# Optimization experiments

Hardware: AMD Instinct MI355X
Metric: run time of the kernel (lower is better)

The kernel has to match this reference:

```python
import jax, jax.numpy as jnp
import numpy as np

B, N = 128, 512            # graphs per batch, nodes (seq len) per graph
NODE_VOCAB, APP_VOCAB = 30000, 5000
D, R, K = 128, 512, 3      # embed_size, rec_embed dim, Chebyshev order
EPS = 1e-12


def setup_inputs() -> dict:
    key = jax.random.key(0)
    ks = jax.random.split(key, 8)
    return {
        # all tokens nonzero -> every position is a valid node (item > 0 filter passes)
        "input_seq": jax.random.randint(ks[0], (B, N), 1, NODE_VOCAB),
        "recd_token": jax.random.randint(ks[1], (B, N), 1, APP_VOCAB),
        "embed_table": jax.random.normal(ks[2], (NODE_VOCAB, D), jnp.float32) * 0.02,
        "rec_embed_table": jax.random.normal(ks[3], (APP_VOCAB, R), jnp.float32) * 0.02,
        "cheb_w1": jax.random.normal(ks[4], (K, D, D), jnp.float32) / np.sqrt(D),
        "cheb_b1": jnp.zeros((D,), jnp.float32),
        "cheb_w2": jax.random.normal(ks[5], (K, D, D), jnp.float32) / np.sqrt(D),
        "cheb_b2": jnp.zeros((D,), jnp.float32),
    }


def _prop_matrix(app_emb):
    """Per-sample scaled Laplacian L_hat = -D^{-1/2} A D^{-1/2}.

    app_emb: [B,N,R] (detached upstream, matching recd.detach() in the source).
    Adjacency: cosine-sim matrix, entries below the mean of the nonzero strict
    upper triangle zeroed. ChebConv receives edge_index only -> binary weights,
    self-loops removed, default lambda_max=2 -> L_hat = -A_norm.
    """
    app_feat = app_emb / jnp.maximum(
        jnp.linalg.norm(app_emb, axis=-1, keepdims=True), EPS)      # F.normalize dim=1
    A = jnp.einsum('bnr,bmr->bnm', app_feat, app_feat)              # [B,N,N]
    upper = jnp.triu(A, 1)
    cnt = jnp.sum(upper != 0, axis=(1, 2)).astype(A.dtype)
    mean = jnp.sum(upper, axis=(1, 2)) / jnp.maximum(cnt, 1.0)      # [B]
    A = jnp.where(A < mean[:, None, None], 0.0, A)
    adj = (A != 0).astype(A.dtype) * (1.0 - jnp.eye(N, dtype=A.dtype))  # binary, no self-loops
    deg = adj.sum(-1)                                               # [B,N]
    dinv = jnp.where(deg > 0, jax.lax.rsqrt(jnp.maximum(deg, EPS)), 0.0)
    return -(dinv[:, :, None] * adj * dinv[:, None, :])             # [B,N,N]


def _cheb(x, S, w, b):
    # Chebyshev recurrence T0=x, T1=Sx, T2=2S T1 - T0
    tx0 = x
    tx1 = jnp.einsum('bnm,bmd->bnd', S, tx0)
    tx2 = 2.0 * jnp.einsum('bnm,bmd->bnd', S, tx1) - tx0
    return (jnp.einsum('bnd,de->bne', tx0, w[0])
            + jnp.einsum('bnd,de->bne', tx1, w[1])
            + jnp.einsum('bnd,de->bne', tx2, w[2]) + b)


def reference(input_seq, recd_token, embed_table, rec_embed_table,
              cheb_w1, cheb_b1, cheb_w2, cheb_b2):
    app_emb = rec_embed_table[recd_token]                           # [B,N,R]
    # adjacency built from detached embeddings (recd.detach() in source)
    S = jax.lax.stop_gradient(_prop_matrix(jax.lax.stop_gradient(app_emb)))
    x = embed_table[input_seq]                                      # [B,N,D]
    x = jax.nn.relu(_cheb(x, S, cheb_w1, cheb_b1))
    x = jax.nn.relu(_cheb(x, S, cheb_w2, cheb_b2))
    out = jnp.concatenate([x, app_emb], axis=-1)                    # [B,N,D+R]
    return out.reshape(B * N, D + R)                                # Batch'ed node features
```

## Files before the change

### kernel.cpp

```cpp
#include <hip/hip_runtime.h>
#include <hip/hip_bf16.h>

typedef __attribute__((ext_vector_type(8))) unsigned short ushort8;
typedef __attribute__((ext_vector_type(4))) unsigned short bf16x4;
typedef __attribute__((ext_vector_type(8))) short short8;
typedef __attribute__((ext_vector_type(4))) float f32x4;
typedef __attribute__((ext_vector_type(2))) unsigned long long u64x2;

#define DEV __device__ __forceinline__

DEV unsigned short f2bf(float f) {
    unsigned u = __builtin_bit_cast(unsigned, f);
    return (unsigned short)((u + 0x7fffu + ((u >> 16) & 1u)) >> 16);
}
DEV float bf2f(unsigned short h) {
    unsigned u = ((unsigned)h) << 16;
    return __builtin_bit_cast(float, u);
}
DEV float wred(float v) {
#pragma unroll
    for (int m = 32; m > 0; m >>= 1) v += __shfl_xor(v, m, 64);
    return v;
}

constexpr int N_ = 512, D_ = 128, R_ = 512;
constexpr long NN2 = (long)N_ * N_;
constexpr int PSTR = 520;
constexpr int USTR = 136;

DEV void gll16(const void* g, void* l) {
    __builtin_amdgcn_global_load_lds(
        (const __attribute__((address_space(1))) unsigned*)g,
        (__attribute__((address_space(3))) unsigned*)l, 16, 0, 0);
}


__global__ __launch_bounds__(256) void k_front(const int* __restrict__ recd,
                                               const float* __restrict__ rtab,
                                               const int* __restrict__ seq,
                                               const float* __restrict__ etab,
                                               const float* __restrict__ w1,
                                               const float* __restrict__ w2,
                                               float* __restrict__ out,
                                               unsigned short* __restrict__ x,
                                               unsigned short* __restrict__ wT,
                                               unsigned short* __restrict__ rtb,
                                               float* __restrict__ rnorm) {
    int bid = blockIdx.x, tid = threadIdx.x;
    if (bid < 16384) {
        int lane = tid & 63, w = tid >> 6;
        long r = (long)bid * 4 + w;
        int tok = recd[r];
        const float* src = rtab + (long)tok * R_;
        int j = lane * 8;
        float4 v0 = *(const float4*)(src + j);
        float4 v1 = *(const float4*)(src + j + 4);
        float ssq = v0.x*v0.x + v0.y*v0.y + v0.z*v0.z + v0.w*v0.w
                  + v1.x*v1.x + v1.y*v1.y + v1.z*v1.z + v1.w*v1.w;
        ssq = wred(ssq);
        float* o = out + r * 640 + 128 + j;
        *(float4*)o = v0;
        *(float4*)(o + 4) = v1;
        if (lane == 0) rnorm[r] = 1.0f / fmaxf(sqrtf(ssq), 1e-12f);
    } else if (bid < 20480) {
        long e8 = ((long)(bid - 16384) * 256 + tid) * 8;
        long r = e8 >> 7;
        int d0 = (int)(e8 & 127);
        int tok = seq[r];
        const float* src = etab + (long)tok * D_ + d0;
        float4 v0 = *(const float4*)src, v1 = *(const float4*)(src + 4);
        ushort8 u;
        u[0]=f2bf(v0.x); u[1]=f2bf(v0.y); u[2]=f2bf(v0.z); u[3]=f2bf(v0.w);
        u[4]=f2bf(v1.x); u[5]=f2bf(v1.y); u[6]=f2bf(v1.z); u[7]=f2bf(v1.w);
        *(ushort8*)(x + e8) = u;
    } else if (bid < 20864) {
        int o = (bid - 20480) * 256 + tid;
        int l = o / 49152;
        int rr = o - l * 49152;
        int mat = rr >> 14;
        int e2 = rr & 16383;
        int e = e2 >> 7, d = e2 & 127;
        const float* w = l ? w2 : w1;
        float v;
        if (mat == 0)      v = w[d * 128 + e] - w[32768 + d * 128 + e];
        else if (mat == 1) v = w[16384 + d * 128 + e];
        else               v = 2.0f * w[32768 + d * 128 + e];
        wT[o] = f2bf(v);
    } else {
        long e8 = ((long)(bid - 20864) * 256 + tid) * 8;
        float4 v0 = *(const float4*)(rtab + e8), v1 = *(const float4*)(rtab + e8 + 4);
        ushort8 u;
        u[0]=f2bf(v0.x); u[1]=f2bf(v0.y); u[2]=f2bf(v0.z); u[3]=f2bf(v0.w);
        u[4]=f2bf(v1.x); u[5]=f2bf(v1.y); u[6]=f2bf(v1.z); u[7]=f2bf(v1.w);
        *(ushort8*)(rtb + e8) = u;
    }
}


DEV void stage_rowmajor(const unsigned short* base, long ld, int k0,
                        unsigned short* dst, int tid) {
#pragma unroll
    for (int i = 0; i < 4; ++i) {
        int u = i * 256 + tid;
        int r = u >> 3, c = (u & 7) * 8;
        gll16(base + (long)r * ld + k0 + c,
              dst + i * 2048 + (tid & 448) * 8);
    }
}

DEV void stage_gather(const unsigned short* tab, const int* toks, int k0,
                      unsigned short* dst, int tid) {
#pragma unroll
    for (int i = 0; i < 4; ++i) {
        int u = i * 256 + tid;
        int r = u >> 3, c = (u & 7) * 8;
        gll16(tab + (long)toks[r] * 512 + k0 + c,
              dst + i * 2048 + (tid & 448) * 8);
    }
}


DEV void stageA256(const unsigned short* base, int k0, unsigned short* dst, int tid) {
    int w = tid >> 6;
#pragma unroll
    for (int i = 0; i < 4; ++i) {
        int u = i * 512 + tid;
        int r = u >> 3, c = (u & 7) * 8;
        gll16(base + (long)r * 128 + k0 + c, dst + (i * 64 + w * 8) * 64);
    }
}

DEV void stageB128(const unsigned short* base, int k0, unsigned short* dst, int tid) {
    int w = tid >> 6;
#pragma unroll
    for (int i = 0; i < 2; ++i) {
        int u = i * 512 + tid;
        int r = u >> 3, c = (u & 7) * 8;
        gll16(base + (long)r * 128 + k0 + c, dst + (i * 64 + w * 8) * 64);
    }
}


__global__ __launch_bounds__(256) void k_adj(const unsigned short* __restrict__ rtb,
                                             const int* __restrict__ recd,
                                             const float* __restrict__ rnorm,
                                             unsigned short* __restrict__ Abf,
                                             float* __restrict__ psum,
                                             float* __restrict__ pcnt) {
    __shared__ __align__(16) unsigned short As[128 * 64], Bs[128 * 64];
    __shared__ int toks[256];
    __shared__ float sred[4], cred[4];
    int g = blockIdx.x;
    int r8 = g & 7, q = g >> 3;
    int q10 = q / 10;
    int b = r8 + (q10 << 3);
    int t = q - q10 * 10;
    int tm = (t < 4) ? 0 : (t < 7) ? 1 : (t < 9) ? 2 : 3;
    int tn = t - (tm * (9 - tm)) / 2 + tm;
    bool diag = (tm == tn);
    int tid = threadIdx.x, lane = tid & 63, wave = tid >> 6;
    if (tid < 128) toks[tid] = recd[b * 512 + tm * 128 + tid];
    else           toks[tid] = recd[b * 512 + tn * 128 + (tid - 128)];
    int wm = wave >> 1, wn = wave & 1;
    int fr = lane & 15, ko = (lane >> 4) * 8;
    f32x4 acc[4][4] = {};
    for (int k0 = 0; k0 < 512; k0 += 64) {
        __syncthreads();
        stage_gather(rtb, toks, k0, As, tid);
        if (!diag) stage_gather(rtb, toks + 128, k0, Bs, tid);
        __syncthreads();
        const unsigned short* Bsrc = diag ? As : Bs;
#pragma unroll
        for (int ks = 0; ks < 2; ++ks) {
            short8 a[4], bb[4];
#pragma unroll
            for (int m = 0; m < 4; ++m)
                a[m] = *(const short8*)(As + (wm * 64 + m * 16 + fr) * 64 + ks * 32 + ko);
#pragma unroll
            for (int n = 0; n < 4; ++n)
                bb[n] = *(const short8*)(Bsrc + (wn * 64 + n * 16 + fr) * 64 + ks * 32 + ko);
#pragma unroll
            for (int m = 0; m < 4; ++m)
#pragma unroll
                for (int n = 0; n < 4; ++n)
                    acc[m][n] = __builtin_amdgcn_mfma_f32_16x16x32_bf16(
                        a[m], bb[n], acc[m][n], 0, 0, 0);
        }
    }
    float s = 0.f, c = 0.f;
    unsigned short* Ab = Abf + (long)b * NN2;
    const float* rnb = rnorm + (long)b * 512;
#pragma unroll
    for (int m = 0; m < 4; ++m) {
        int gi0 = tm * 128 + wm * 64 + m * 16 + (lane >> 4) * 4;
        float4 rni = *(const float4*)(rnb + gi0);
#pragma unroll
        for (int n = 0; n < 4; ++n) {
            int gj = tn * 128 + wn * 64 + n * 16 + fr;
            float rj = rnb[gj];
            f32x4 v = acc[m][n];
            bf16x4 tw;
#pragma unroll
            for (int qq = 0; qq < 4; ++qq) {
                int gi = gi0 + qq;
                float vv = v[qq] * (&rni.x)[qq] * rj;
                unsigned short bv = f2bf(vv);
                Ab[(long)gi * N_ + gj] = bv;
                tw[qq] = bv;
                if (gj > gi) {
                    s += vv;
                    c += (vv != 0.0f) ? 1.0f : 0.0f;
                }
            }
            if (!diag)
                *(bf16x4*)(Ab + (long)gj * N_ + gi0) = tw;
        }
    }
    s = wred(s);
    c = wred(c);
    if (lane == 0) { sred[wave] = s; cred[wave] = c; }
    __syncthreads();
    if (tid == 0) {
        psum[b * 16 + t] = sred[0] + sred[1] + sred[2] + sred[3];
        pcnt[b * 16 + t] = cred[0] + cred[1] + cred[2] + cred[3];
    }
}

__global__ __launch_bounds__(256) void k_degtrs(unsigned short* __restrict__ Abf,
                                                const float* __restrict__ psum,
                                                const float* __restrict__ pcnt,
                                                const unsigned short* __restrict__ xin,
                                                float* __restrict__ dinv,
                                                unsigned short* __restrict__ pT) {
    __shared__ unsigned char mb[4][64];
    __shared__ float sdinv[64];
    __shared__ unsigned short t[64 * 128];
    int bid = blockIdx.x;
    int q = bid >> 3, r8 = bid & 7;
    int b = r8 + ((q >> 3) << 3);
    int tn = q & 7;
    int tid = threadIdx.x, lane = tid & 63, w = tid >> 6;
    float s = 0.f, c = 0.f;
#pragma unroll
    for (int k = 0; k < 10; ++k) { s += psum[b * 16 + k]; c += pcnt[b * 16 + k]; }
    float m = s / fmaxf(c, 1.0f);
#pragma unroll 1
    for (int i = 0; i < 16; ++i) {
        int rl = w * 16 + i;
        long r = (long)b * 512 + tn * 64 + rl;
        int ig = tn * 64 + rl;
        ushort8 v = *(const ushort8*)(Abf + r * 512 + lane * 8);
        unsigned byt = 0;
        int cnt = 0;
#pragma unroll
        for (int k = 0; k < 8; ++k) {
            float f = bf2f(v[k]);
            int j = lane * 8 + k;
            bool keep = (f >= m) && (f != 0.0f) && (j != ig);
            byt |= (keep ? 1u : 0u) << k;
            cnt += keep ? 1 : 0;
        }
        mb[w][lane] = (unsigned char)byt;
        float fc = wred((float)cnt);
        if (lane < 8) {
            unsigned long long mword = *(const unsigned long long*)&mb[w][lane * 8];
            *(unsigned long long*)((unsigned char*)Abf + r * 1024 + lane * 8) = mword;
        }
        if (lane == 8) {
            float dv = (fc > 0.f) ? rsqrtf(fc) : 0.f;
            dinv[r] = dv;
            sdinv[rl] = dv;
        }
    }
    __syncthreads();
    const unsigned short* ib = xin + ((long)b * 512 + tn * 64) * 128;
    unsigned short* ob = pT + (long)b * 65536 + tn * 64;
#pragma unroll
    for (int i = 0; i < 4; ++i) {
        int u = i * 256 + tid;
        int n = u >> 4, g = u & 15;
        float sc = sdinv[n];
        ushort8 v = *(const ushort8*)(ib + n * 128 + g * 8);
        ushort8 sv;
#pragma unroll
        for (int tt = 0; tt < 8; ++tt) sv[tt] = f2bf(bf2f(v[tt]) * sc);
        int gs = g ^ ((n >> 3) & 7);
        *(ushort8*)(t + n * 128 + gs * 8) = sv;
    }
    __syncthreads();
#pragma unroll
    for (int i = 0; i < 4; ++i) {
        int u = i * 256 + tid;
        int d = u >> 3, n8 = (u & 7) * 8;
        ushort8 v;
#pragma unroll
        for (int tt = 0; tt < 8; ++tt) {
            int n = n8 + tt;
            int g = (d >> 3) ^ ((n >> 3) & 7);
            v[tt] = t[n * 128 + g * 8 + (d & 7)];
        }
        *(ushort8*)(ob + (long)d * 512 + n8) = v;
    }
}

__global__ __launch_bounds__(512) void k_sxm(const unsigned short* __restrict__ Abf,
                                             const float* __restrict__ dinv,
                                             const unsigned short* __restrict__ pT,
                                             unsigned short* __restrict__ outN,
                                             unsigned short* __restrict__ outT) {
    __shared__ __align__(16) unsigned short Ps[128 * PSTR];
    __shared__ __align__(8) unsigned short lut4[16 * 4];
    int tid = threadIdx.x, lane = tid & 63, w = tid >> 6;
    if (tid < 16) {
        unsigned long long e = 0;
#pragma unroll
        for (int j = 0; j < 4; ++j)
            if ((tid >> j) & 1) e |= 0x3F80ull << (16 * j);
        *(unsigned long long*)(lut4 + tid * 4) = e;
    }
    int g = blockIdx.x;
    int xcd = g & 7, idx = g >> 3;
    int b = xcd + ((idx >> 1) << 3);
    int half = idx & 1;
    int wm = w >> 1, wn = w & 1;
    int fr = lane & 15, ko = (lane >> 4) * 8;
    const unsigned char* mbase = (const unsigned char*)Abf + (long)b * 524288;
    const unsigned short* pb = pT + (long)b * 65536;
#pragma unroll
    for (int i = 0; i < 16; ++i) {
        int r = i * 8 + w;
        gll16(pb + (long)r * 512 + lane * 8, Ps + r * PSTR);
    }
    __syncthreads();
    f32x4 acc[4][4] = {};
    int rowbase = half * 256 + wm * 64;
#pragma unroll 1
    for (int k0 = 0; k0 < 512; k0 += 128) {
        u64x2 mw[4];
#pragma unroll
        for (int m = 0; m < 4; ++m) {
            int row = rowbase + m * 16 + fr;
            mw[m] = *(const u64x2*)(mbase + (long)row * 1024 + (k0 >> 3));
        }
#pragma unroll
        for (int kss = 0; kss < 4; ++kss) {
            short8 a4[4], b4[4];
#pragma unroll
            for (int m = 0; m < 4; ++m) {
                unsigned w32 = (unsigned)(mw[m][kss >> 1] >> ((kss & 1) * 32));
                unsigned byt = (w32 >> ko) & 255u;
                unsigned long long lo = *(const unsigned long long*)(lut4 + (byt & 15u) * 4);
                unsigned long long hi = *(const unsigned long long*)(lut4 + (byt >> 4) * 4);
                u64x2 tt; tt[0] = lo; tt[1] = hi;
                a4[m] = __builtin_bit_cast(short8, tt);
            }
#pragma unroll
            for (int n = 0; n < 4; ++n)
                b4[n] = *(const short8*)(Ps + (wn * 64 + n * 16 + fr) * PSTR + k0 + kss * 32 + ko);
#pragma unroll
            for (int m = 0; m < 4; ++m)
#pragma unroll
                for (int n = 0; n < 4; ++n)
                    acc[m][n] = __builtin_amdgcn_mfma_f32_16x16x32_bf16(
                        a4[m], b4[n], acc[m][n], 0, 0, 0);
        }
    }
    unsigned short* on = outN + (long)b * 65536;
#pragma unroll
    for (int m = 0; m < 4; ++m) {
        int gi0 = half * 256 + wm * 64 + m * 16 + ((lane >> 4) << 2);
        float4 dv = *(const float4*)(dinv + (long)b * 512 + gi0);
#pragma unroll
        for (int n = 0; n < 4; ++n) {
            int gj = wn * 64 + n * 16 + fr;
            bf16x4 tw;
#pragma unroll
            for (int qq = 0; qq < 4; ++qq) {
                float dq = (&dv.x)[qq];
                float t1v = -dq * acc[m][n][qq];
                on[(long)(gi0 + qq) * 128 + gj] = f2bf(t1v);
                tw[qq] = f2bf(dq * t1v);
            }
            *(bf16x4*)(outT + (long)b * 65536 + (long)gj * 512 + gi0) = tw;
        }
    }
}

template <int LAYER>
__global__ __launch_bounds__(512) void k_sxp(const unsigned short* __restrict__ Abf,
                                             const float* __restrict__ dinv,
                                             const unsigned short* __restrict__ pTin,
                                             const unsigned short* __restrict__ t0,
                                             const unsigned short* __restrict__ t1,
                                             const unsigned short* __restrict__ wTl,
                                             const float* __restrict__ bias,
                                             unsigned short* __restrict__ ybf,
                                             unsigned short* __restrict__ pTout,
                                             float* __restrict__ out) {
    __shared__ __align__(16) unsigned short lds[128 * PSTR];
    __shared__ __align__(8) unsigned short lut4[16 * 4];
    int tid = threadIdx.x, lane = tid & 63, w = tid >> 6;
    if (tid < 16) {
        unsigned long long e = 0;
#pragma unroll
        for (int j = 0; j < 4; ++j)
            if ((tid >> j) & 1) e |= 0x3F80ull << (16 * j);
        *(unsigned long long*)(lut4 + tid * 4) = e;
    }
    int g = blockIdx.x;
    int xcd = g & 7, idx = g >> 3;
    int b = xcd + ((idx >> 1) << 3);
    int half = idx & 1;
    int wm = w >> 1, wn = w & 1;
    int fr = lane & 15, ko = (lane >> 4) * 8;
    unsigned short* As  = lds;
    unsigned short* Bs  = lds + 16384;
    unsigned short* uL  = lds + 24576;
    {
        const unsigned char* mbase = (const unsigned char*)Abf + (long)b * 524288;
        const unsigned short* pb = pTin + (long)b * 65536;
#pragma unroll
        for (int i = 0; i < 16; ++i) {
            int r = i * 8 + w;
            gll16(pb + (long)r * 512 + lane * 8, lds + r * PSTR);
        }
        __syncthreads();
        f32x4 acc[4][4] = {};
        int rowbase = half * 256 + wm * 64;
#pragma unroll 1
        for (int k0 = 0; k0 < 512; k0 += 128) {
            u64x2 mw[4];
#pragma unroll
            for (int m = 0; m < 4; ++m) {
                int row = rowbase + m * 16 + fr;
                mw[m] = *(const u64x2*)(mbase + (long)row * 1024 + (k0 >> 3));
            }
#pragma unroll
            for (int kss = 0; kss < 4; ++kss) {
                short8 a4[4], b4[4];
#pragma unroll
                for (int m = 0; m < 4; ++m) {
                    unsigned w32 = (unsigned)(mw[m][kss >> 1] >> ((kss & 1) * 32));
                    unsigned byt = (w32 >> ko) & 255u;
                    unsigned long long lo = *(const unsigned long long*)(lut4 + (byt & 15u) * 4);
                    unsigned long long hi = *(const unsigned long long*)(lut4 + (byt >> 4) * 4);
                    u64x2 tt; tt[0] = lo; tt[1] = hi;
                    a4[m] = __builtin_bit_cast(short8, tt);
                }
#pragma unroll
                for (int n = 0; n < 4; ++n)
                    b4[n] = *(const short8*)(lds + (wn * 64 + n * 16 + fr) * PSTR + k0 + kss * 32 + ko);
#pragma unroll
                for (int m = 0; m < 4; ++m)
#pragma unroll
                    for (int n = 0; n < 4; ++n)
                        acc[m][n] = __builtin_amdgcn_mfma_f32_16x16x32_bf16(
                            a4[m], b4[n], acc[m][n], 0, 0, 0);
            }
        }
        __syncthreads();
#pragma unroll
        for (int m = 0; m < 4; ++m) {
            int li0 = wm * 64 + m * 16 + ((lane >> 4) << 2);
            float4 dv = *(const float4*)(dinv + (long)b * 512 + half * 256 + li0);
#pragma unroll
            for (int n = 0; n < 4; ++n) {
                int gj = wn * 64 + n * 16 + fr;
#pragma unroll
                for (int qq = 0; qq < 4; ++qq)
                    uL[(li0 + qq) * USTR + gj] = f2bf(-(&dv.x)[qq] * acc[m][n][qq]);
            }
        }
    }
    long row0 = (long)b * 512 + half * 256;
    f32x4 acc2[4][4] = {};
#pragma unroll 1
    for (int mat = 0; mat < 2; ++mat) {
        const unsigned short* tsrc = (mat == 0) ? (t0 + row0 * D_) : (t1 + row0 * D_);
        const unsigned short* wsrc = wTl + mat * 16384;
#pragma unroll 1
        for (int k0 = 0; k0 < 128; k0 += 64) {
            __syncthreads();
            stageA256(tsrc, k0, As, tid);
            stageB128(wsrc, k0, Bs, tid);
            __syncthreads();
#pragma unroll
            for (int ks = 0; ks < 2; ++ks) {
                short8 a[4], bfr[4];
#pragma unroll
                for (int m = 0; m < 4; ++m)
                    a[m] = *(const short8*)(As + (wm * 64 + m * 16 + fr) * 64 + ks * 32 + ko);
#pragma unroll
                for (int n = 0; n < 4; ++n)
                    bfr[n] = *(const short8*)(Bs + (wn * 64 + n * 16 + fr) * 64 + ks * 32 + ko);
#pragma unroll
                for (int m = 0; m < 4; ++m)
#pragma unroll
                    for (int n = 0; n < 4; ++n)
                        acc2[m][n] = __builtin_amdgcn_mfma_f32_16x16x32_bf16(
                            a[m], bfr[n], acc2[m][n], 0, 0, 0);
            }
        }
    }
#pragma unroll 1
    for (int s2 = 0; s2 < 2; ++s2) {
        __syncthreads();
        stageB128(wTl + 32768, s2 * 64, Bs, tid);
        __syncthreads();
#pragma unroll
        for (int ks = 0; ks < 2; ++ks) {
            short8 a[4], bfr[4];
#pragma unroll
            for (int m = 0; m < 4; ++m)
                a[m] = *(const short8*)(uL + (wm * 64 + m * 16 + fr) * USTR + s2 * 64 + ks * 32 + ko);
#pragma unroll
            for (int n = 0; n < 4; ++n)
                bfr[n] = *(const short8*)(Bs + (wn * 64 + n * 16 + fr) * 64 + ks * 32 + ko);
#pragma unroll
            for (int m = 0; m < 4; ++m)
#pragma unroll
                for (int n = 0; n < 4; ++n)
                    acc2[m][n] = __builtin_amdgcn_mfma_f32_16x16x32_bf16(
                        a[m], bfr[n], acc2[m][n], 0, 0, 0);
        }
    }
#pragma unroll
    for (int m = 0; m < 4; ++m) {
        long gr0 = row0 + wm * 64 + m * 16 + ((lane >> 4) << 2);
        float4 dv;
        if (LAYER == 1) dv = *(const float4*)(dinv + gr0);
#pragma unroll
        for (int n = 0; n < 4; ++n) {
            int gj = wn * 64 + n * 16 + (lane & 15);
            bf16x4 tw;
#pragma unroll
            for (int qq = 0; qq < 4; ++qq) {
                long gr = gr0 + qq;
                float v = fmaxf(acc2[m][n][qq] + bias[gj], 0.0f);
                if (LAYER == 1) {
                    ybf[gr * D_ + gj] = f2bf(v);
                    tw[qq] = f2bf((&dv.x)[qq] * v);
                } else {
                    out[gr * 640 + gj] = v;
                }
            }
            if (LAYER == 1)
                *(bf16x4*)(pTout + (gr0 >> 9) * 65536 + (long)gj * 512 + (gr0 & 511)) = tw;
        }
    }
}


extern "C" void kernel_launch(void* const* d_in, const int* in_sizes, int n_in,
                              void* d_out, int out_size, void* d_ws, size_t ws_size,
                              hipStream_t stream) {
    const int* seq    = (const int*)d_in[0];
    const int* recd   = (const int*)d_in[1];
    const float* etab = (const float*)d_in[2];
    const float* rtab = (const float*)d_in[3];
    const float* w1   = (const float*)d_in[4];
    const float* b1   = (const float*)d_in[5];
    const float* w2   = (const float*)d_in[6];
    const float* b2   = (const float*)d_in[7];
    float* out = (float*)d_out;
    char* ws = (char*)d_ws;

    if (ws_size < 151470592u) return;

    unsigned short* Abf  = (unsigned short*)(ws);
    unsigned short* pTa  = (unsigned short*)(ws + 67108864);
    unsigned short* pTb  = (unsigned short*)(ws + 83886080);
    unsigned short* t1   = (unsigned short*)(ws + 100663296);
    unsigned short* rtb  = (unsigned short*)(ws + 117440512);
    float* rnorm         = (float*)(ws + 122683392);
    unsigned short* xbf  = (unsigned short*)(ws + 134217728);
    unsigned short* wT   = (unsigned short*)(ws + 150994944);
    float* psum = (float*)(ws + 151191552);
    float* pcnt = (float*)(ws + 151199744);
    float* dinv = (float*)(ws + 151208448);

    k_front<<<22114, 256, 0, stream>>>(recd, rtab, seq, etab, w1, w2,
                                       out, xbf, wT, rtb, rnorm);
    k_adj<<<1280, 256, 0, stream>>>(rtb, recd, rnorm, Abf, psum, pcnt);
    k_degtrs<<<1024, 256, 0, stream>>>(Abf, psum, pcnt, xbf, dinv, pTa);
    k_sxm<<<256, 512, 0, stream>>>(Abf, dinv, pTa, t1, pTb);
    k_sxp<1><<<256, 512, 0, stream>>>(Abf, dinv, pTb, xbf, t1, wT, b1,
                                      xbf, pTa, nullptr);
    k_sxm<<<256, 512, 0, stream>>>(Abf, dinv, pTa, t1, pTb);
    k_sxp<2><<<256, 512, 0, stream>>>(Abf, dinv, pTb, xbf, t1, wT + 49152, b2,
                                      nullptr, nullptr, out);
}
```

Before: 222.9 us.

## Load MFMA operands directly from global memory instead of staging through LDS

In the adjacency kernel, the off-diagonal B operand is now read straight from the gathered embedding table into registers, which drops the second LDS tile and its staging. In the Chebyshev layer kernel, the dense feature and weight GEMMs read A and B fragments directly from global memory rather than staging them through LDS, removing several barriers and the As/Bs buffers. This cuts LDS footprint and synchronisation but turns coalesced block loads into strided per-lane 16-byte global reads, relying on L2/L1 caching, which may raise memory latency.

```diff
diff --git a/kernel.cpp b/kernel.cpp
--- a/kernel.cpp
+++ b/kernel.cpp
@@ -97,17 +97,6 @@
 }
 
 
-DEV void stage_rowmajor(const unsigned short* base, long ld, int k0,
-                        unsigned short* dst, int tid) {
-#pragma unroll
-    for (int i = 0; i < 4; ++i) {
-        int u = i * 256 + tid;
-        int r = u >> 3, c = (u & 7) * 8;
-        gll16(base + (long)r * ld + k0 + c,
-              dst + i * 2048 + (tid & 448) * 8);
-    }
-}
-
 DEV void stage_gather(const unsigned short* tab, const int* toks, int k0,
                       unsigned short* dst, int tid) {
 #pragma unroll
@@ -116,27 +105,6 @@
         int r = u >> 3, c = (u & 7) * 8;
         gll16(tab + (long)toks[r] * 512 + k0 + c,
               dst + i * 2048 + (tid & 448) * 8);
-    }
-}
-
-
-DEV void stageA256(const unsigned short* base, int k0, unsigned short* dst, int tid) {
-    int w = tid >> 6;
-#pragma unroll
-    for (int i = 0; i < 4; ++i) {
-        int u = i * 512 + tid;
-        int r = u >> 3, c = (u & 7) * 8;
-        gll16(base + (long)r * 128 + k0 + c, dst + (i * 64 + w * 8) * 64);
-    }
-}
-
-DEV void stageB128(const unsigned short* base, int k0, unsigned short* dst, int tid) {
-    int w = tid >> 6;
-#pragma unroll
-    for (int i = 0; i < 2; ++i) {
-        int u = i * 512 + tid;
-        int r = u >> 3, c = (u & 7) * 8;
-        gll16(base + (long)r * 128 + k0 + c, dst + (i * 64 + w * 8) * 64);
     }
 }
 
@@ -147,7 +115,7 @@
                                              unsigned short* __restrict__ Abf,
                                              float* __restrict__ psum,
                                              float* __restrict__ pcnt) {
-    __shared__ __align__(16) unsigned short As[128 * 64], Bs[128 * 64];
+    __shared__ __align__(16) unsigned short As[128 * 64];
     __shared__ int toks[256];
     __shared__ float sred[4], cred[4];
     int g = blockIdx.x;
@@ -163,13 +131,16 @@
     else           toks[tid] = recd[b * 512 + tn * 128 + (tid - 128)];
     int wm = wave >> 1, wn = wave & 1;
     int fr = lane & 15, ko = (lane >> 4) * 8;
+    __syncthreads();
+    int tokB[4];
+#pragma unroll
+    for (int n = 0; n < 4; ++n)
+        tokB[n] = toks[128 + wn * 64 + n * 16 + fr];
     f32x4 acc[4][4] = {};
     for (int k0 = 0; k0 < 512; k0 += 64) {
         __syncthreads();
         stage_gather(rtb, toks, k0, As, tid);
-        if (!diag) stage_gather(rtb, toks + 128, k0, Bs, tid);
         __syncthreads();
-        const unsigned short* Bsrc = diag ? As : Bs;
 #pragma unroll
         for (int ks = 0; ks < 2; ++ks) {
             short8 a[4], bb[4];
@@ -177,8 +148,12 @@
             for (int m = 0; m < 4; ++m)
                 a[m] = *(const short8*)(As + (wm * 64 + m * 16 + fr) * 64 + ks * 32 + ko);
 #pragma unroll
-            for (int n = 0; n < 4; ++n)
-                bb[n] = *(const short8*)(Bsrc + (wn * 64 + n * 16 + fr) * 64 + ks * 32 + ko);
+            for (int n = 0; n < 4; ++n) {
+                if (diag)
+                    bb[n] = *(const short8*)(As + (wn * 64 + n * 16 + fr) * 64 + ks * 32 + ko);
+                else
+                    bb[n] = *(const short8*)(rtb + (long)tokB[n] * 512 + k0 + ks * 32 + ko);
+            }
 #pragma unroll
             for (int m = 0; m < 4; ++m)
 #pragma unroll
@@ -413,9 +388,7 @@
     int half = idx & 1;
     int wm = w >> 1, wn = w & 1;
     int fr = lane & 15, ko = (lane >> 4) * 8;
-    unsigned short* As  = lds;
-    unsigned short* Bs  = lds + 16384;
-    unsigned short* uL  = lds + 24576;
+    unsigned short* uL = lds;
     {
         const unsigned char* mbase = (const unsigned char*)Abf + (long)b * 524288;
         const unsigned short* pb = pTin + (long)b * 65536;
@@ -471,51 +444,23 @@
                     uL[(li0 + qq) * USTR + gj] = f2bf(-(&dv.x)[qq] * acc[m][n][qq]);
             }
         }
+        __syncthreads();
     }
     long row0 = (long)b * 512 + half * 256;
     f32x4 acc2[4][4] = {};
 #pragma unroll 1
     for (int mat = 0; mat < 2; ++mat) {
-        const unsigned short* tsrc = (mat == 0) ? (t0 + row0 * D_) : (t1 + row0 * D_);
+        const unsigned short* tsrc = (mat == 0) ? t0 : t1;
         const unsigned short* wsrc = wTl + mat * 16384;
-#pragma unroll 1
-        for (int k0 = 0; k0 < 128; k0 += 64) {
-            __syncthreads();
-            stageA256(tsrc, k0, As, tid);
-            stageB128(wsrc, k0, Bs, tid);
-            __syncthreads();
-#pragma unroll
-            for (int ks = 0; ks < 2; ++ks) {
-                short8 a[4], bfr[4];
-#pragma unroll
-                for (int m = 0; m < 4; ++m)
-                    a[m] = *(const short8*)(As + (wm * 64 + m * 16 + fr) * 64 + ks * 32 + ko);
-#pragma unroll
-                for (int n = 0; n < 4; ++n)
-                    bfr[n] = *(const short8*)(Bs + (wn * 64 + n * 16 + fr) * 64 + ks * 32 + ko);
-#pragma unroll
-                for (int m = 0; m < 4; ++m)
-#pragma unroll
-                    for (int n = 0; n < 4; ++n)
-                        acc2[m][n] = __builtin_amdgcn_mfma_f32_16x16x32_bf16(
-                            a[m], bfr[n], acc2[m][n], 0, 0, 0);
-            }
-        }
-    }
-#pragma unroll 1
-    for (int s2 = 0; s2 < 2; ++s2) {
-        __syncthreads();
-        stageB128(wTl + 32768, s2 * 64, Bs, tid);
-        __syncthreads();
-#pragma unroll
-        for (int ks = 0; ks < 2; ++ks) {
+#pragma unroll
+        for (int kk = 0; kk < 4; ++kk) {
             short8 a[4], bfr[4];
 #pragma unroll
             for (int m = 0; m < 4; ++m)
-                a[m] = *(const short8*)(uL + (wm * 64 + m * 16 + fr) * USTR + s2 * 64 + ks * 32 + ko);
+                a[m] = *(const short8*)(tsrc + (row0 + wm * 64 + m * 16 + fr) * D_ + kk * 32 + ko);
 #pragma unroll
             for (int n = 0; n < 4; ++n)
-                bfr[n] = *(const short8*)(Bs + (wn * 64 + n * 16 + fr) * 64 + ks * 32 + ko);
+                bfr[n] = *(const short8*)(wsrc + (wn * 64 + n * 16 + fr) * 128 + kk * 32 + ko);
 #pragma unroll
             for (int m = 0; m < 4; ++m)
 #pragma unroll
@@ -523,6 +468,22 @@
                     acc2[m][n] = __builtin_amdgcn_mfma_f32_16x16x32_bf16(
                         a[m], bfr[n], acc2[m][n], 0, 0, 0);
         }
+    }
+#pragma unroll
+    for (int kk = 0; kk < 4; ++kk) {
+        short8 a[4], bfr[4];
+#pragma unroll
+        for (int m = 0; m < 4; ++m)
+            a[m] = *(const short8*)(uL + (wm * 64 + m * 16 + fr) * USTR + kk * 32 + ko);
+#pragma unroll
+        for (int n = 0; n < 4; ++n)
+            bfr[n] = *(const short8*)(wTl + 32768 + (wn * 64 + n * 16 + fr) * 128 + kk * 32 + ko);
+#pragma unroll
+        for (int m = 0; m < 4; ++m)
+#pragma unroll
+            for (int n = 0; n < 4; ++n)
+                acc2[m][n] = __builtin_amdgcn_mfma_f32_16x16x32_bf16(
+                    a[m], bfr[n], acc2[m][n], 0, 0, 0);
     }
 #pragma unroll
     for (int m = 0; m < 4; ++m) {
```

Measured after the change: 250.6 us (median of 3 runs). 1.12x slower.
